# Kernel optimization log

Measured on AMD Instinct MI355X. Metric: run time of the kernel, lower is better.

The kernel has to match this reference:

```python
import jax, jax.numpy as jnp
import numpy as np

B, T, D = 2, 1024, 2048      # batch, seq, model dim
E, F, K = 64, 512, 4          # n_experts, expert hidden, top-k
S, HS = 2, 512 * 4            # shared experts, shared hidden = expert_dim * topk


def setup_inputs() -> dict:
    key = jax.random.key(0)
    ks = jax.random.split(key, 9)
    s = 0.02
    f32 = jnp.float32
    return {
        "x": jax.random.normal(ks[0], (B, T, D), f32),
        "router_w": jax.random.normal(ks[1], (D, E), f32) * s,
        "router_bias": jnp.zeros((E,), f32),
        "wg": jax.random.normal(ks[2], (E, D, F), f32) * s,
        "wu": jax.random.normal(ks[3], (E, D, F), f32) * s,
        "wd": jax.random.normal(ks[4], (E, F, D), f32) * s,
        "swg": jax.random.normal(ks[5], (S, D, HS), f32) * s,
        "swu": jax.random.normal(ks[6], (S, D, HS), f32) * s,
        "swd": jax.random.normal(ks[7], (S, HS, D), f32) * s,
    }


def reference(x, router_w, router_bias, wg, wu, wd, swg, swu, swd):
    b, t, d = x.shape
    flat = x.reshape(b * t, d)                      # [N, D]
    n = flat.shape[0]

    # Router: softmax scores, top-k selection on (logits + bias)
    logits = flat @ router_w                         # [N, E]
    scores = jax.nn.softmax(logits, axis=-1)
    _, topk_idx = jax.lax.top_k(logits + router_bias, K)          # [N, K]
    topk_scores = jnp.take_along_axis(scores, topk_idx, axis=-1)  # [N, K]
    topk_scores = topk_scores / topk_scores.sum(axis=-1, keepdims=True)

    # Dense combine weights: w[n, e] = normalized score if expert e selected else 0
    comb = jnp.zeros((n, E), dtype=flat.dtype).at[
        jnp.arange(n)[:, None], topk_idx].set(topk_scores)        # [N, E]

    # Routed experts (SwiGLU), computed densely and masked by combine weights
    g = jax.nn.silu(jnp.einsum('nd,edf->nef', flat, wg))          # [N, E, F]
    u = jnp.einsum('nd,edf->nef', flat, wu)                       # [N, E, F]
    routed = jnp.einsum('ne,nef,efd->nd', comb, g * u, wd)        # [N, D]

    # Shared experts (always active, summed)
    sg = jax.nn.silu(jnp.einsum('nd,sdh->nsh', flat, swg))        # [N, S, HS]
    su = jnp.einsum('nd,sdh->nsh', flat, swu)
    shared = jnp.einsum('nsh,shd->nd', sg * su, swd)              # [N, D]

    return (routed + shared).reshape(b, t, d)
```

## Files before the change

kernel.cpp:

```cpp
#include <hip/hip_runtime.h>
#include <hip/hip_bf16.h>

typedef __bf16 bf16x8 __attribute__((ext_vector_type(8)));
typedef float f32x4 __attribute__((ext_vector_type(4)));
typedef unsigned short u16x4 __attribute__((ext_vector_type(4)));
typedef unsigned short u16x8 __attribute__((ext_vector_type(8)));

#define DEVI __device__ __forceinline__

constexpr int N_TOK = 2048;
constexpr int DIM   = 2048;
constexpr int NEXP  = 64;
constexpr int FDIM  = 512;
constexpr int TOPK  = 4;
constexpr int NSH   = 2;
constexpr int HSH   = 2048;

#define WAIT_VM0 asm volatile("s_waitcnt vmcnt(0)" ::: "memory")
#define WAIT_VM3 asm volatile("s_waitcnt vmcnt(3)" ::: "memory")
#define WAIT_VM4 asm volatile("s_waitcnt vmcnt(4)" ::: "memory")
#define WAIT_VM6 asm volatile("s_waitcnt vmcnt(6)" ::: "memory")
#define WAIT_LG0 asm volatile("s_waitcnt lgkmcnt(0)" ::: "memory")
#define SBAR __builtin_amdgcn_s_barrier()

DEVI unsigned short f2b(float f) {
  union { float fv; unsigned u; } v; v.fv = f;
  unsigned r = v.u + 0x7fffu + ((v.u >> 16) & 1u);
  return (unsigned short)(r >> 16);
}
DEVI float b2f(unsigned short h) {
  union { unsigned u; float f; } v; v.u = ((unsigned)h) << 16;
  return v.f;
}
DEVI void gll16(const void* g, void* l) {
  __builtin_amdgcn_global_load_lds((const __attribute__((address_space(1))) unsigned*)g,
                                   (__attribute__((address_space(3))) unsigned*)l, 16, 0, 0);
}
DEVI unsigned cvtpk(float lo, float hi) {
  unsigned r;
  asm("v_cvt_pk_bf16_f32 %0, %1, %2" : "=v"(r) : "v"(lo), "v"(hi));
  return r;
}
DEVI bf16x8 fragB(const float* base, int str) {
  union { unsigned u[4]; bf16x8 v; } r;
  #pragma unroll
  for (int p = 0; p < 4; ++p) r.u[p] = cvtpk(base[(2 * p) * str], base[(2 * p + 1) * str]);
  return r.v;
}

__global__ void cvt_x_kernel(const float* __restrict__ x, unsigned short* __restrict__ xb) {
  const size_t i = ((size_t)blockIdx.x * 256 + threadIdx.x) * 8;
  const float4 a = *reinterpret_cast<const float4*>(x + i);
  const float4 b = *reinterpret_cast<const float4*>(x + i + 4);
  u16x8 o;
  o[0] = f2b(a.x); o[1] = f2b(a.y); o[2] = f2b(a.z); o[3] = f2b(a.w);
  o[4] = f2b(b.x); o[5] = f2b(b.y); o[6] = f2b(b.z); o[7] = f2b(b.w);
  *reinterpret_cast<u16x8*>(xb + i) = o;
}

__global__ __launch_bounds__(256)
void tr_shared_kernel(const float* __restrict__ swu, const float* __restrict__ swg,
                      const float* __restrict__ swd, unsigned short* __restrict__ swuT,
                      unsigned short* __restrict__ swgT, unsigned short* __restrict__ swdT) {
  __shared__ float Lf[64][68];
  const int tid = threadIdx.x;
  const int r0 = blockIdx.x * 64, c0 = blockIdx.y * 64;
  const int z = blockIdx.z, mat = z >> 1;
  const size_t soff = (size_t)(z & 1) * DIM * HSH;
  const float* in = (mat == 0 ? swu : mat == 1 ? swg : swd) + soff;
  unsigned short* ot = (mat == 0 ? swuT : mat == 1 ? swgT : swdT) + soff;
  #pragma unroll
  for (int j = 0; j < 4; ++j) {
    const int idx = j * 1024 + tid * 4;
    const int row = idx >> 6, col = idx & 63;
    const float4 v = *reinterpret_cast<const float4*>(in + (size_t)(r0 + row) * 2048 + c0 + col);
    *reinterpret_cast<float4*>(&Lf[row][col]) = v;
  }
  __syncthreads();
  #pragma unroll
  for (int j = 0; j < 4; ++j) {
    const int idx = j * 1024 + tid * 4;
    const int orow = idx >> 6, ocol = idx & 63;
    u16x4 o;
    o[0] = f2b(Lf[ocol][orow]);     o[1] = f2b(Lf[ocol + 1][orow]);
    o[2] = f2b(Lf[ocol + 2][orow]); o[3] = f2b(Lf[ocol + 3][orow]);
    *reinterpret_cast<u16x4*>(ot + (size_t)(c0 + orow) * 2048 + r0 + ocol) = o;
  }
}

__global__ __launch_bounds__(256)
void router_kernel(const float* __restrict__ x, const float* __restrict__ rw,
                   const float* __restrict__ rb, int* __restrict__ cnt,
                   int* __restrict__ listTok, float* __restrict__ listW,
                   int* __restrict__ tokEP) {
  __shared__ float Lx[8][128];
  const int tid = threadIdx.x;
  const int lane = tid & 63;
  const int wave = tid >> 6;
  const int tokBase = blockIdx.x * 8;

  float acc0 = 0.f, acc1 = 0.f;
  for (int dc = 0; dc < DIM; dc += 128) {
    __syncthreads();
    {
      const int idx = tid * 4;
      const int row = idx >> 7, col = idx & 127;
      *reinterpret_cast<float4*>(&Lx[row][col]) =
          *reinterpret_cast<const float4*>(x + (size_t)(tokBase + row) * DIM + dc + col);
    }
    __syncthreads();
    #pragma unroll 16
    for (int dd = 0; dd < 128; ++dd) {
      const float r = rw[(size_t)(dc + dd) * NEXP + lane];
      acc0 = fmaf(Lx[wave * 2 + 0][dd], r, acc0);
      acc1 = fmaf(Lx[wave * 2 + 1][dd], r, acc1);
    }
  }

  const float bias = rb[lane];
  #pragma unroll
  for (int t = 0; t < 2; ++t) {
    const float v = (t == 0) ? acc0 : acc1;
    const int token = tokBase + wave * 2 + t;
    float m = v;
    #pragma unroll
    for (int o = 32; o > 0; o >>= 1) m = fmaxf(m, __shfl_xor(m, o));
    const float p = expf(v - m);
    float ss = p;
    #pragma unroll
    for (int o = 32; o > 0; o >>= 1) ss += __shfl_xor(ss, o);
    const float score = p / ss;
    float cur = v + bias;
    float wk[TOPK]; int ik[TOPK]; float wsum = 0.f;
    #pragma unroll
    for (int k = 0; k < TOPK; ++k) {
      float tm = cur;
      #pragma unroll
      for (int o = 32; o > 0; o >>= 1) tm = fmaxf(tm, __shfl_xor(tm, o));
      const unsigned long long msk = __ballot(cur == tm);
      const int sel = (int)__builtin_ctzll(msk);
      const float w = __shfl(score, sel);
      wk[k] = w; ik[k] = sel; wsum += w;
      if (lane == sel) cur = -3.4e38f;
    }
    if (lane < TOPK) {
      const int e = ik[lane];
      const float w = wk[lane] / wsum;
      const int slot = atomicAdd(&cnt[e], 1);
      listTok[(size_t)e * N_TOK + slot] = token;
      listW[(size_t)e * N_TOK + slot] = w;
      tokEP[token * TOPK + lane] = (e << 16) | slot;
    }
  }
}

__global__ void scan_kernel(const int* __restrict__ cnt, int* __restrict__ off) {
  if (threadIdx.x == 0) {
    int s = 0;
    for (int e = 0; e < NEXP; ++e) { off[e] = s; s += cnt[e]; }
  }
}

__global__ __launch_bounds__(256, 3)
void up_routed(const unsigned short* __restrict__ xb,
               const float* __restrict__ Wu, const float* __restrict__ Wg,
               const int* __restrict__ cnt, const int* __restrict__ off,
               const int* __restrict__ listTok, const float* __restrict__ listW,
               unsigned short* __restrict__ H) {
  constexpr int NT = DIM / 32;
  const int tid = threadIdx.x;
  const int f0 = blockIdx.x * 64;
  const int e  = blockIdx.y;
  const int m0 = blockIdx.z * 128;
  const int c = cnt[e];
  if (m0 >= c) return;
  const int rcnt = min(128, c - m0);
  const int rowbase = off[e] + m0;

  __shared__ __align__(16) unsigned short Al[2][4][128][8];
  __shared__ __align__(16) float Bf[2][2][32][64];
  __shared__ float wSs[128];

  if (tid < 128) wSs[tid] = (tid < rcnt) ? listW[(size_t)e * N_TOK + m0 + tid] : 0.f;
  WAIT_LG0;

  const int wid = tid >> 6, l = tid & 63;
  const int wm = wid >> 1, wn = wid & 1;
  const int lc = l & 15, hi = l >> 4;

  const int t0 = listTok[(size_t)e * N_TOK + m0 + min(l, rcnt - 1)];
  const int t1 = listTok[(size_t)e * N_TOK + m0 + min(64 + l, rcnt - 1)];
  const unsigned short* pa0 = xb + (size_t)t0 * DIM;
  const unsigned short* pa1 = xb + (size_t)t1 * DIM;
  const unsigned short* pas = (wid & 1) ? pa1 : pa0;
  const float* pbu = Wu + (size_t)e * DIM * FDIM + (size_t)(l >> 4) * FDIM + f0 + (l & 15) * 4;
  const float* pbg = Wg + (size_t)e * DIM * FDIM + (size_t)(l >> 4) * FDIM + f0 + (l & 15) * 4;

  auto stage = [&](int g, int b) {
    const int d0 = g * 32;
    gll16(pas + d0 + (wid >> 1) * 8,      &Al[b][wid >> 1][(wid & 1) * 64][0]);
    gll16(pas + d0 + (wid >> 1) * 8 + 16, &Al[b][(wid >> 1) + 2][(wid & 1) * 64][0]);
    gll16(pbu + (size_t)(d0 + 4 * wid) * FDIM,      &Bf[b][0][4 * wid][0]);
    gll16(pbu + (size_t)(d0 + 4 * wid + 16) * FDIM, &Bf[b][0][4 * wid + 16][0]);
    gll16(pbg + (size_t)(d0 + 4 * wid) * FDIM,      &Bf[b][1][4 * wid][0]);
    gll16(pbg + (size_t)(d0 + 4 * wid + 16) * FDIM, &Bf[b][1][4 * wid + 16][0]);
  };

  f32x4 aU[4][2], aG[4][2];
  #pragma unroll
  for (int i = 0; i < 4; ++i)
    #pragma unroll
    for (int j = 0; j < 2; ++j) { aU[i][j] = f32x4{0,0,0,0}; aG[i][j] = f32x4{0,0,0,0}; }

  stage(0, 0);
  for (int g = 0; g < NT; ++g) {
    const int b = g & 1;
    if (g + 1 < NT) { stage(g + 1, b ^ 1); WAIT_VM6; } else { WAIT_VM0; }
    SBAR;
    bf16x8 af[4];
    #pragma unroll
    for (int mi = 0; mi < 4; ++mi)
      af[mi] = *reinterpret_cast<const bf16x8*>(&Al[b][hi][wm * 64 + mi * 16 + lc][0]);
    #pragma unroll
    for (int ni = 0; ni < 2; ++ni) {
      const bf16x8 bu = fragB(&Bf[b][0][hi * 8][wn * 32 + ni * 16 + lc], 64);
      const bf16x8 bg = fragB(&Bf[b][1][hi * 8][wn * 32 + ni * 16 + lc], 64);
      #pragma unroll
      for (int mi = 0; mi < 4; ++mi) {
        aU[mi][ni] = __builtin_amdgcn_mfma_f32_16x16x32_bf16(af[mi], bu, aU[mi][ni], 0, 0, 0);
        aG[mi][ni] = __builtin_amdgcn_mfma_f32_16x16x32_bf16(af[mi], bg, aG[mi][ni], 0, 0, 0);
      }
    }
    SBAR;
  }

  #pragma unroll
  for (int mi = 0; mi < 4; ++mi)
    #pragma unroll
    for (int ni = 0; ni < 2; ++ni)
      #pragma unroll
      for (int r2 = 0; r2 < 4; ++r2) {
        const int row = wm * 64 + mi * 16 + hi * 4 + r2;
        if (row < rcnt) {
          const int col = f0 + wn * 32 + ni * 16 + lc;
          const float g = aG[mi][ni][r2], u = aU[mi][ni][r2];
          const float h = (g / (1.f + __expf(-g))) * u * wSs[row];
          H[(size_t)(rowbase + row) * FDIM + col] = f2b(h);
        }
      }
}

__global__ __launch_bounds__(256, 3)
void down_routed(const unsigned short* __restrict__ Hr, const float* __restrict__ wd,
                 const int* __restrict__ cnt, const int* __restrict__ off,
                 unsigned short* __restrict__ P) {
  constexpr int NT = FDIM / 32;
  const int tid = threadIdx.x;
  const int x0 = blockIdx.x * 128;
  const int e  = blockIdx.y;
  const int m0 = blockIdx.z * 128;
  const int c = cnt[e];
  if (m0 >= c) return;
  const int rcnt = min(128, c - m0);
  const int rowbase = off[e] + m0;

  __shared__ __align__(16) unsigned short Al[2][4][128][8];
  __shared__ __align__(16) float Bf[2][32][128];

  const int wid = tid >> 6, l = tid & 63;
  const int wm = wid >> 1, wn = wid & 1;
  const int lc = l & 15, hi = l >> 4;

  const unsigned short* pa0 = Hr + (size_t)(rowbase + min(l, rcnt - 1)) * FDIM;
  const unsigned short* pa1 = Hr + (size_t)(rowbase + min(64 + l, rcnt - 1)) * FDIM;
  const unsigned short* pas = (wid & 1) ? pa1 : pa0;
  const float* pB = wd + (size_t)e * FDIM * DIM + (size_t)(l >> 5) * DIM + x0 + (l & 31) * 4;

  auto stage = [&](int g, int b) {
    const int d0 = g * 32;
    gll16(pas + d0 + (wid >> 1) * 8,      &Al[b][wid >> 1][(wid & 1) * 64][0]);
    gll16(pas + d0 + (wid >> 1) * 8 + 16, &Al[b][(wid >> 1) + 2][(wid & 1) * 64][0]);
    #pragma unroll
    for (int cc = 0; cc < 4; ++cc) {
      const int i = cc * 4 + wid;
      gll16(pB + (size_t)(d0 + 2 * i) * DIM, &Bf[b][2 * i][0]);
    }
  };

  f32x4 acc[4][4];
  #pragma unroll
  for (int i = 0; i < 4; ++i)
    #pragma unroll
    for (int j = 0; j < 4; ++j) acc[i][j] = f32x4{0,0,0,0};

  stage(0, 0);
  for (int g = 0; g < NT; ++g) {
    const int b = g & 1;
    if (g + 1 < NT) { stage(g + 1, b ^ 1); WAIT_VM6; } else { WAIT_VM0; }
    SBAR;
    bf16x8 af[4];
    #pragma unroll
    for (int mi = 0; mi < 4; ++mi)
      af[mi] = *reinterpret_cast<const bf16x8*>(&Al[b][hi][wm * 64 + mi * 16 + lc][0]);
    #pragma unroll
    for (int ni = 0; ni < 4; ++ni) {
      const bf16x8 bq = fragB(&Bf[b][hi * 8][wn * 64 + ni * 16 + lc], 128);
      #pragma unroll
      for (int mi = 0; mi < 4; ++mi)
        acc[mi][ni] = __builtin_amdgcn_mfma_f32_16x16x32_bf16(af[mi], bq, acc[mi][ni], 0, 0, 0);
    }
    SBAR;
  }

  #pragma unroll
  for (int mi = 0; mi < 4; ++mi)
    #pragma unroll
    for (int ni = 0; ni < 4; ++ni)
      #pragma unroll
      for (int r2 = 0; r2 < 4; ++r2) {
        const int row = wm * 64 + mi * 16 + hi * 4 + r2;
        if (row < rcnt) {
          const int col = x0 + wn * 64 + ni * 16 + lc;
          P[(size_t)(rowbase + row) * DIM + col] = f2b(acc[mi][ni][r2]);
        }
      }
}

__global__ __launch_bounds__(256, 4)
void up_shared(const unsigned short* __restrict__ xb,
               const unsigned short* __restrict__ WuT, const unsigned short* __restrict__ WgT,
               unsigned short* __restrict__ H) {
  constexpr int NT = DIM / 32;
  const int tid = threadIdx.x;
  const int f0 = blockIdx.x * 64;
  const int s  = blockIdx.y;
  const int m0 = blockIdx.z * 128;

  __shared__ __align__(16) unsigned short Al[2][4][128][8];
  __shared__ __align__(16) unsigned short Bu[2][4][64][8];
  __shared__ __align__(16) unsigned short Bg[2][4][64][8];

  const int wid = tid >> 6, l = tid & 63;
  const int wm = wid >> 1, wn = wid & 1;
  const int lc = l & 15, hi = l >> 4;

  const unsigned short* pa0 = xb + (size_t)(m0 + l) * DIM;
  const unsigned short* pa1 = xb + (size_t)(m0 + 64 + l) * DIM;
  const unsigned short* pas = (wid & 1) ? pa1 : pa0;
  const unsigned short* pbu = WuT + (size_t)s * HSH * DIM + (size_t)(f0 + l) * DIM;
  const unsigned short* pbg = WgT + (size_t)s * HSH * DIM + (size_t)(f0 + l) * DIM;

  auto stage = [&](int g, int b) {
    const int d0 = g * 32;
    gll16(pas + d0 + (wid >> 1) * 8,      &Al[b][wid >> 1][(wid & 1) * 64][0]);
    gll16(pas + d0 + (wid >> 1) * 8 + 16, &Al[b][(wid >> 1) + 2][(wid & 1) * 64][0]);
    gll16(pbu + d0 + wid * 8, &Bu[b][wid][0][0]);
    gll16(pbg + d0 + wid * 8, &Bg[b][wid][0][0]);
  };

  f32x4 aU[4][2], aG[4][2];
  #pragma unroll
  for (int i = 0; i < 4; ++i)
    #pragma unroll
    for (int j = 0; j < 2; ++j) { aU[i][j] = f32x4{0,0,0,0}; aG[i][j] = f32x4{0,0,0,0}; }

  stage(0, 0);
  for (int g = 0; g < NT; ++g) {
    const int b = g & 1;
    if (g + 1 < NT) { stage(g + 1, b ^ 1); WAIT_VM4; } else { WAIT_VM0; }
    SBAR;
    bf16x8 af[4], bu[2], bg[2];
    #pragma unroll
    for (int mi = 0; mi < 4; ++mi)
      af[mi] = *reinterpret_cast<const bf16x8*>(&Al[b][hi][wm * 64 + mi * 16 + lc][0]);
    #pragma unroll
    for (int ni = 0; ni < 2; ++ni) {
      bu[ni] = *reinterpret_cast<const bf16x8*>(&Bu[b][hi][wn * 32 + ni * 16 + lc][0]);
      bg[ni] = *reinterpret_cast<const bf16x8*>(&Bg[b][hi][wn * 32 + ni * 16 + lc][0]);
    }
    #pragma unroll
    for (int mi = 0; mi < 4; ++mi)
      #pragma unroll
      for (int ni = 0; ni < 2; ++ni) {
        aU[mi][ni] = __builtin_amdgcn_mfma_f32_16x16x32_bf16(af[mi], bu[ni], aU[mi][ni], 0, 0, 0);
        aG[mi][ni] = __builtin_amdgcn_mfma_f32_16x16x32_bf16(af[mi], bg[ni], aG[mi][ni], 0, 0, 0);
      }
    SBAR;
  }

  #pragma unroll
  for (int mi = 0; mi < 4; ++mi)
    #pragma unroll
    for (int ni = 0; ni < 2; ++ni)
      #pragma unroll
      for (int r2 = 0; r2 < 4; ++r2) {
        const int row = wm * 64 + mi * 16 + hi * 4 + r2;
        const int col = f0 + wn * 32 + ni * 16 + lc;
        const float g = aG[mi][ni][r2], u = aU[mi][ni][r2];
        H[((size_t)s * N_TOK + m0 + row) * HSH + col] = f2b((g / (1.f + __expf(-g))) * u);
      }
}

__global__ __launch_bounds__(256, 4)
void down_shared(const unsigned short* __restrict__ Hs, const unsigned short* __restrict__ swdT,
                 float* __restrict__ out) {
  constexpr int NT = 2 * HSH / 32;
  const int tid = threadIdx.x;
  const int x0 = blockIdx.x * 128;
  const int m0 = blockIdx.z * 64;

  __shared__ __align__(16) unsigned short Al[2][4][64][8];
  __shared__ __align__(16) unsigned short Bl[2][4][128][8];

  const int wid = tid >> 6, l = tid & 63;
  const int wm = wid >> 1, wn = wid & 1;
  const int lc = l & 15, hi = l >> 4;

  const unsigned short* paA = Hs + (size_t)(m0 + l) * HSH;
  const unsigned short* pb0 = swdT + (size_t)(x0 + l) * HSH;
  const unsigned short* pb1 = swdT + (size_t)(x0 + 64 + l) * HSH;
  const unsigned short* pbs = (wid & 1) ? pb1 : pb0;

  auto stage = [&](int g, int b) {
    const int seg = g >> 6;
    const int dk = (g & 63) * 32;
    const size_t aoff = (size_t)seg * N_TOK * HSH;
    const size_t boff = (size_t)seg * HSH * DIM;
    gll16(paA + aoff + dk + wid * 8, &Al[b][wid][0][0]);
    gll16(pbs + boff + dk + (wid >> 1) * 8,      &Bl[b][wid >> 1][(wid & 1) * 64][0]);
    gll16(pbs + boff + dk + (wid >> 1) * 8 + 16, &Bl[b][(wid >> 1) + 2][(wid & 1) * 64][0]);
  };

  f32x4 acc[2][4];
  #pragma unroll
  for (int i = 0; i < 2; ++i)
    #pragma unroll
    for (int j = 0; j < 4; ++j) acc[i][j] = f32x4{0,0,0,0};

  stage(0, 0);
  for (int g = 0; g < NT; ++g) {
    const int b = g & 1;
    if (g + 1 < NT) { stage(g + 1, b ^ 1); WAIT_VM3; } else { WAIT_VM0; }
    SBAR;
    bf16x8 af[2], bq[4];
    #pragma unroll
    for (int mi = 0; mi < 2; ++mi)
      af[mi] = *reinterpret_cast<const bf16x8*>(&Al[b][hi][wm * 32 + mi * 16 + lc][0]);
    #pragma unroll
    for (int ni = 0; ni < 4; ++ni)
      bq[ni] = *reinterpret_cast<const bf16x8*>(&Bl[b][hi][wn * 64 + ni * 16 + lc][0]);
    #pragma unroll
    for (int mi = 0; mi < 2; ++mi)
      #pragma unroll
      for (int ni = 0; ni < 4; ++ni)
        acc[mi][ni] = __builtin_amdgcn_mfma_f32_16x16x32_bf16(af[mi], bq[ni], acc[mi][ni], 0, 0, 0);
    SBAR;
  }

  #pragma unroll
  for (int mi = 0; mi < 2; ++mi)
    #pragma unroll
    for (int ni = 0; ni < 4; ++ni)
      #pragma unroll
      for (int r2 = 0; r2 < 4; ++r2) {
        const int row = wm * 32 + mi * 16 + hi * 4 + r2;
        const int col = x0 + wn * 64 + ni * 16 + lc;
        out[(size_t)(m0 + row) * DIM + col] = acc[mi][ni][r2];
      }
}

__global__ __launch_bounds__(256)
void combine_kernel(const int* __restrict__ tokEP, const int* __restrict__ off,
                    const unsigned short* __restrict__ P, float* __restrict__ out) {
  const int n = blockIdx.x;
  const int tid = threadIdx.x;
  int rows[4];
  #pragma unroll
  for (int k = 0; k < TOPK; ++k) {
    const int ep = tokEP[n * TOPK + k];
    rows[k] = off[ep >> 16] + (ep & 0xffff);
  }
  const int cc = tid * 8;
  float* po = out + (size_t)n * DIM + cc;
  float4 o0 = *reinterpret_cast<const float4*>(po);
  float4 o1 = *reinterpret_cast<const float4*>(po + 4);
  #pragma unroll
  for (int k = 0; k < TOPK; ++k) {
    const u16x8 v = *reinterpret_cast<const u16x8*>(P + (size_t)rows[k] * DIM + cc);
    o0.x += b2f(v[0]); o0.y += b2f(v[1]); o0.z += b2f(v[2]); o0.w += b2f(v[3]);
    o1.x += b2f(v[4]); o1.y += b2f(v[5]); o1.z += b2f(v[6]); o1.w += b2f(v[7]);
  }
  *reinterpret_cast<float4*>(po) = o0;
  *reinterpret_cast<float4*>(po + 4) = o1;
}

extern "C" void kernel_launch(void* const* d_in, const int* in_sizes, int n_in,
                              void* d_out, int out_size, void* d_ws, size_t ws_size,
                              hipStream_t stream) {
  const float* x   = (const float*)d_in[0];
  const float* rw  = (const float*)d_in[1];
  const float* rb  = (const float*)d_in[2];
  const float* wg  = (const float*)d_in[3];
  const float* wu  = (const float*)d_in[4];
  const float* wd  = (const float*)d_in[5];
  const float* swg = (const float*)d_in[6];
  const float* swu = (const float*)d_in[7];
  const float* swd = (const float*)d_in[8];
  float* out = (float*)d_out;
  char* ws = (char*)d_ws;

  int* cnt = (int*)ws;
  int* off = (int*)(ws + 256);
  int* tokEP = (int*)(ws + 4096);
  int* listTok = (int*)(ws + 64 * 1024);
  float* listW = (float*)(ws + 576 * 1024);
  unsigned short* xb   = (unsigned short*)(ws + (size_t) 2 * 1024 * 1024);
  unsigned short* Hr   = (unsigned short*)(ws + (size_t)10 * 1024 * 1024);
  unsigned short* Hs   = (unsigned short*)(ws + (size_t)18 * 1024 * 1024);
  unsigned short* swuT = (unsigned short*)(ws + (size_t)34 * 1024 * 1024);
  unsigned short* swgT = (unsigned short*)(ws + (size_t)50 * 1024 * 1024);
  unsigned short* swdT = (unsigned short*)(ws + (size_t)66 * 1024 * 1024);
  unsigned short* P    = (unsigned short*)(ws + (size_t)82 * 1024 * 1024);

  hipMemsetAsync(cnt, 0, NEXP * sizeof(int), stream);
  cvt_x_kernel<<<(N_TOK * DIM) / (256 * 8), 256, 0, stream>>>(x, xb);
  tr_shared_kernel<<<dim3(32, 32, 6), 256, 0, stream>>>(swu, swg, swd, swuT, swgT, swdT);
  router_kernel<<<N_TOK / 8, 256, 0, stream>>>(x, rw, rb, cnt, listTok, listW, tokEP);
  scan_kernel<<<1, 64, 0, stream>>>(cnt, off);

  up_routed<<<dim3(FDIM / 64, NEXP, 16), 256, 0, stream>>>(
      xb, wu, wg, cnt, off, listTok, listW, Hr);
  up_shared<<<dim3(HSH / 64, NSH, N_TOK / 128), 256, 0, stream>>>(
      xb, swuT, swgT, Hs);
  down_shared<<<dim3(DIM / 128, 1, N_TOK / 64), 256, 0, stream>>>(
      Hs, swdT, out);
  down_routed<<<dim3(DIM / 128, NEXP, 16), 256, 0, stream>>>(
      Hr, wd, cnt, off, P);
  combine_kernel<<<N_TOK, 256, 0, stream>>>(tokEP, off, P, out);
}
```

Baseline: 717.4 us.

## Restructure routed GEMMs with register-staged bf16 weights and triple-buffer shared GEMMs

The routed up-projection is split into two passes, first up then gate, and each pass covers 256 rows per block so every weight tile is shared by twice as many tokens. The fp32 routed weights are now loaded into registers, converted to bf16 once, and written to LDS. This removes the per-fragment fp32-to-bf16 conversion that ran inside the MFMA loop. The down-routed kernel gets the same treatment with 64-column tiles, and the shared-expert GEMMs switch from double to triple buffering. Kernel launch order also changes. The costs are an extra read-modify-write of H in the gate pass and higher LDS and register pressure.

```diff
diff --git a/kernel.cpp b/kernel.cpp
--- a/kernel.cpp
+++ b/kernel.cpp
@@ -3,6 +3,8 @@
 
 typedef __bf16 bf16x8 __attribute__((ext_vector_type(8)));
 typedef float f32x4 __attribute__((ext_vector_type(4)));
+typedef float f32x2 __attribute__((ext_vector_type(2)));
+typedef unsigned short u16x2 __attribute__((ext_vector_type(2)));
 typedef unsigned short u16x4 __attribute__((ext_vector_type(4)));
 typedef unsigned short u16x8 __attribute__((ext_vector_type(8)));
 
@@ -17,9 +19,11 @@
 constexpr int HSH   = 2048;
 
 #define WAIT_VM0 asm volatile("s_waitcnt vmcnt(0)" ::: "memory")
+#define WAIT_VM2 asm volatile("s_waitcnt vmcnt(2)" ::: "memory")
 #define WAIT_VM3 asm volatile("s_waitcnt vmcnt(3)" ::: "memory")
 #define WAIT_VM4 asm volatile("s_waitcnt vmcnt(4)" ::: "memory")
 #define WAIT_VM6 asm volatile("s_waitcnt vmcnt(6)" ::: "memory")
+#define WAIT_VM8 asm volatile("s_waitcnt vmcnt(8)" ::: "memory")
 #define WAIT_LG0 asm volatile("s_waitcnt lgkmcnt(0)" ::: "memory")
 #define SBAR __builtin_amdgcn_s_barrier()
 
@@ -35,17 +39,6 @@
 DEVI void gll16(const void* g, void* l) {
   __builtin_amdgcn_global_load_lds((const __attribute__((address_space(1))) unsigned*)g,
                                    (__attribute__((address_space(3))) unsigned*)l, 16, 0, 0);
-}
-DEVI unsigned cvtpk(float lo, float hi) {
-  unsigned r;
-  asm("v_cvt_pk_bf16_f32 %0, %1, %2" : "=v"(r) : "v"(lo), "v"(hi));
-  return r;
-}
-DEVI bf16x8 fragB(const float* base, int str) {
-  union { unsigned u[4]; bf16x8 v; } r;
-  #pragma unroll
-  for (int p = 0; p < 4; ++p) r.u[p] = cvtpk(base[(2 * p) * str], base[(2 * p + 1) * str]);
-  return r.v;
 }
 
 __global__ void cvt_x_kernel(const float* __restrict__ x, unsigned short* __restrict__ xb) {
@@ -161,9 +154,9 @@
   }
 }
 
+template<bool GPASS>
 __global__ __launch_bounds__(256, 3)
-void up_routed(const unsigned short* __restrict__ xb,
-               const float* __restrict__ Wu, const float* __restrict__ Wg,
+void up_routed(const unsigned short* __restrict__ xb, const float* __restrict__ W,
                const int* __restrict__ cnt, const int* __restrict__ off,
                const int* __restrict__ listTok, const float* __restrict__ listW,
                unsigned short* __restrict__ H) {
@@ -171,83 +164,127 @@
   const int tid = threadIdx.x;
   const int f0 = blockIdx.x * 64;
   const int e  = blockIdx.y;
-  const int m0 = blockIdx.z * 128;
+  const int m0 = blockIdx.z * 256;
   const int c = cnt[e];
   if (m0 >= c) return;
-  const int rcnt = min(128, c - m0);
+  const int rc0 = min(128, c - m0);
+  const int rc1 = min(128, max(0, c - m0 - 128));
   const int rowbase = off[e] + m0;
 
-  __shared__ __align__(16) unsigned short Al[2][4][128][8];
-  __shared__ __align__(16) float Bf[2][2][32][64];
-  __shared__ float wSs[128];
-
-  if (tid < 128) wSs[tid] = (tid < rcnt) ? listW[(size_t)e * N_TOK + m0 + tid] : 0.f;
-  WAIT_LG0;
+  __shared__ __align__(16) unsigned short Al[2][2][4][128][8];
+  __shared__ __align__(16) unsigned short Bb[2][4][64][8];
+  __shared__ float wSs[256];
+
+  if (GPASS) wSs[tid] = (m0 + tid < c) ? listW[(size_t)e * N_TOK + m0 + tid] : 0.f;
 
   const int wid = tid >> 6, l = tid & 63;
   const int wm = wid >> 1, wn = wid & 1;
   const int lc = l & 15, hi = l >> 4;
 
-  const int t0 = listTok[(size_t)e * N_TOK + m0 + min(l, rcnt - 1)];
-  const int t1 = listTok[(size_t)e * N_TOK + m0 + min(64 + l, rcnt - 1)];
-  const unsigned short* pa0 = xb + (size_t)t0 * DIM;
-  const unsigned short* pa1 = xb + (size_t)t1 * DIM;
-  const unsigned short* pas = (wid & 1) ? pa1 : pa0;
-  const float* pbu = Wu + (size_t)e * DIM * FDIM + (size_t)(l >> 4) * FDIM + f0 + (l & 15) * 4;
-  const float* pbg = Wg + (size_t)e * DIM * FDIM + (size_t)(l >> 4) * FDIM + f0 + (l & 15) * 4;
-
-  auto stage = [&](int g, int b) {
-    const int d0 = g * 32;
-    gll16(pas + d0 + (wid >> 1) * 8,      &Al[b][wid >> 1][(wid & 1) * 64][0]);
-    gll16(pas + d0 + (wid >> 1) * 8 + 16, &Al[b][(wid >> 1) + 2][(wid & 1) * 64][0]);
-    gll16(pbu + (size_t)(d0 + 4 * wid) * FDIM,      &Bf[b][0][4 * wid][0]);
-    gll16(pbu + (size_t)(d0 + 4 * wid + 16) * FDIM, &Bf[b][0][4 * wid + 16][0]);
-    gll16(pbg + (size_t)(d0 + 4 * wid) * FDIM,      &Bf[b][1][4 * wid][0]);
-    gll16(pbg + (size_t)(d0 + 4 * wid + 16) * FDIM, &Bf[b][1][4 * wid + 16][0]);
-  };
-
-  f32x4 aU[4][2], aG[4][2];
+  const unsigned short* pa[4];
+  #pragma unroll
+  for (int j = 0; j < 4; ++j) {
+    const int tok = listTok[(size_t)e * N_TOK + min(m0 + j * 64 + l, c - 1)];
+    pa[j] = xb + (size_t)tok * DIM;
+  }
+  const float* pw = W + (size_t)e * DIM * FDIM + f0 + (tid & 15) * 4;
+  const int ko = tid >> 4;
+
+  f32x4 rb0[2], rb1[2];
+  f32x4 a0[4][2], a1[4][2];
   #pragma unroll
   for (int i = 0; i < 4; ++i)
     #pragma unroll
-    for (int j = 0; j < 2; ++j) { aU[i][j] = f32x4{0,0,0,0}; aG[i][j] = f32x4{0,0,0,0}; }
-
-  stage(0, 0);
-  for (int g = 0; g < NT; ++g) {
-    const int b = g & 1;
-    if (g + 1 < NT) { stage(g + 1, b ^ 1); WAIT_VM6; } else { WAIT_VM0; }
-    SBAR;
-    bf16x8 af[4];
+    for (int j = 0; j < 2; ++j) { a0[i][j] = f32x4{0,0,0,0}; a1[i][j] = f32x4{0,0,0,0}; }
+
+#define UPR_STAGEA(G, B_) do { const int d0_ = (G) * 32;            \
+    gll16(pa[0] + d0_ + wid * 8, &Al[B_][0][wid][0][0]);            \
+    gll16(pa[1] + d0_ + wid * 8, &Al[B_][0][wid][64][0]);           \
+    gll16(pa[2] + d0_ + wid * 8, &Al[B_][1][wid][0][0]);            \
+    gll16(pa[3] + d0_ + wid * 8, &Al[B_][1][wid][64][0]); } while (0)
+
+#define UPR_LOADB(G, R) do { const int d0_ = (G) * 32;                                    \
+    R[0] = *reinterpret_cast<const f32x4*>(pw + (size_t)(d0_ + 2 * ko) * FDIM);           \
+    R[1] = *reinterpret_cast<const f32x4*>(pw + (size_t)(d0_ + 2 * ko + 1) * FDIM); } while (0)
+
+#define UPR_WRITEB(R, B_) do {                                                            \
+    _Pragma("unroll")                                                                     \
+    for (int cc = 0; cc < 4; ++cc) {                                                      \
+      u16x2 v2; v2[0] = f2b(R[0][cc]); v2[1] = f2b(R[1][cc]);                             \
+      *reinterpret_cast<u16x2*>(&Bb[B_][ko >> 2][(tid & 15) * 4 + cc][2 * (ko & 3)]) = v2;\
+    } } while (0)
+
+#define UPR_COMPUTE(B_) do {                                                              \
+    const bf16x8 bq0 = *reinterpret_cast<const bf16x8*>(&Bb[B_][hi][wn * 32 + lc][0]);    \
+    const bf16x8 bq1 = *reinterpret_cast<const bf16x8*>(&Bb[B_][hi][wn * 32 + 16 + lc][0]);\
+    _Pragma("unroll")                                                                     \
+    for (int mi = 0; mi < 4; ++mi) {                                                      \
+      const bf16x8 af = *reinterpret_cast<const bf16x8*>(&Al[B_][0][hi][wm * 64 + mi * 16 + lc][0]); \
+      a0[mi][0] = __builtin_amdgcn_mfma_f32_16x16x32_bf16(af, bq0, a0[mi][0], 0, 0, 0);   \
+      a0[mi][1] = __builtin_amdgcn_mfma_f32_16x16x32_bf16(af, bq1, a0[mi][1], 0, 0, 0);   \
+    }                                                                                     \
+    _Pragma("unroll")                                                                     \
+    for (int mi = 0; mi < 4; ++mi) {                                                      \
+      const bf16x8 af = *reinterpret_cast<const bf16x8*>(&Al[B_][1][hi][wm * 64 + mi * 16 + lc][0]); \
+      a1[mi][0] = __builtin_amdgcn_mfma_f32_16x16x32_bf16(af, bq0, a1[mi][0], 0, 0, 0);   \
+      a1[mi][1] = __builtin_amdgcn_mfma_f32_16x16x32_bf16(af, bq1, a1[mi][1], 0, 0, 0);   \
+    } } while (0)
+
+  UPR_LOADB(0, rb0);
+  UPR_STAGEA(0, 0);
+  UPR_LOADB(1, rb1);
+  WAIT_VM6;
+  UPR_WRITEB(rb0, 0);
+  WAIT_VM2;
+  WAIT_LG0; SBAR;
+
+  for (int t = 0; t < NT - 2; t += 2) {
+    UPR_STAGEA(t + 1, 1);
+    UPR_LOADB(t + 2, rb0);
+    WAIT_VM6; UPR_WRITEB(rb1, 1);
+    UPR_COMPUTE(0);
+    WAIT_VM2; WAIT_LG0; SBAR;
+    UPR_STAGEA(t + 2, 0);
+    UPR_LOADB(t + 3, rb1);
+    WAIT_VM6; UPR_WRITEB(rb0, 0);
+    UPR_COMPUTE(1);
+    WAIT_VM2; WAIT_LG0; SBAR;
+  }
+  UPR_STAGEA(NT - 1, 1);
+  WAIT_VM4;
+  UPR_WRITEB(rb1, 1);
+  UPR_COMPUTE(0);
+  WAIT_VM0; WAIT_LG0; SBAR;
+  UPR_COMPUTE(1);
+
+#undef UPR_STAGEA
+#undef UPR_LOADB
+#undef UPR_WRITEB
+#undef UPR_COMPUTE
+
+  #pragma unroll
+  for (int tile = 0; tile < 2; ++tile) {
+    const int rc = tile ? rc1 : rc0;
     #pragma unroll
     for (int mi = 0; mi < 4; ++mi)
-      af[mi] = *reinterpret_cast<const bf16x8*>(&Al[b][hi][wm * 64 + mi * 16 + lc][0]);
-    #pragma unroll
-    for (int ni = 0; ni < 2; ++ni) {
-      const bf16x8 bu = fragB(&Bf[b][0][hi * 8][wn * 32 + ni * 16 + lc], 64);
-      const bf16x8 bg = fragB(&Bf[b][1][hi * 8][wn * 32 + ni * 16 + lc], 64);
       #pragma unroll
-      for (int mi = 0; mi < 4; ++mi) {
-        aU[mi][ni] = __builtin_amdgcn_mfma_f32_16x16x32_bf16(af[mi], bu, aU[mi][ni], 0, 0, 0);
-        aG[mi][ni] = __builtin_amdgcn_mfma_f32_16x16x32_bf16(af[mi], bg, aG[mi][ni], 0, 0, 0);
-      }
-    }
-    SBAR;
-  }
-
-  #pragma unroll
-  for (int mi = 0; mi < 4; ++mi)
-    #pragma unroll
-    for (int ni = 0; ni < 2; ++ni)
-      #pragma unroll
-      for (int r2 = 0; r2 < 4; ++r2) {
-        const int row = wm * 64 + mi * 16 + hi * 4 + r2;
-        if (row < rcnt) {
-          const int col = f0 + wn * 32 + ni * 16 + lc;
-          const float g = aG[mi][ni][r2], u = aU[mi][ni][r2];
-          const float h = (g / (1.f + __expf(-g))) * u * wSs[row];
-          H[(size_t)(rowbase + row) * FDIM + col] = f2b(h);
+      for (int ni = 0; ni < 2; ++ni)
+        #pragma unroll
+        for (int r2 = 0; r2 < 4; ++r2) {
+          const int row = wm * 64 + mi * 16 + hi * 4 + r2;
+          if (row < rc) {
+            const int col = f0 + wn * 32 + ni * 16 + lc;
+            const size_t idx = (size_t)(rowbase + tile * 128 + row) * FDIM + col;
+            const float v = tile ? a1[mi][ni][r2] : a0[mi][ni][r2];
+            if (GPASS) {
+              const float u = b2f(H[idx]);
+              H[idx] = f2b((v / (1.f + __expf(-v))) * u * wSs[tile * 128 + row]);
+            } else {
+              H[idx] = f2b(v);
+            }
+          }
         }
-      }
+  }
 }
 
 __global__ __launch_bounds__(256, 3)
@@ -256,77 +293,124 @@
                  unsigned short* __restrict__ P) {
   constexpr int NT = FDIM / 32;
   const int tid = threadIdx.x;
-  const int x0 = blockIdx.x * 128;
+  const int x0 = blockIdx.x * 64;
   const int e  = blockIdx.y;
-  const int m0 = blockIdx.z * 128;
+  const int m0 = blockIdx.z * 256;
   const int c = cnt[e];
   if (m0 >= c) return;
-  const int rcnt = min(128, c - m0);
+  const int rc0 = min(128, c - m0);
+  const int rc1 = min(128, max(0, c - m0 - 128));
   const int rowbase = off[e] + m0;
 
-  __shared__ __align__(16) unsigned short Al[2][4][128][8];
-  __shared__ __align__(16) float Bf[2][32][128];
+  __shared__ __align__(16) unsigned short Al[2][2][4][128][8];
+  __shared__ __align__(16) unsigned short Bb[2][4][64][8];
 
   const int wid = tid >> 6, l = tid & 63;
   const int wm = wid >> 1, wn = wid & 1;
   const int lc = l & 15, hi = l >> 4;
 
-  const unsigned short* pa0 = Hr + (size_t)(rowbase + min(l, rcnt - 1)) * FDIM;
-  const unsigned short* pa1 = Hr + (size_t)(rowbase + min(64 + l, rcnt - 1)) * FDIM;
-  const unsigned short* pas = (wid & 1) ? pa1 : pa0;
-  const float* pB = wd + (size_t)e * FDIM * DIM + (size_t)(l >> 5) * DIM + x0 + (l & 31) * 4;
-
-  auto stage = [&](int g, int b) {
-    const int d0 = g * 32;
-    gll16(pas + d0 + (wid >> 1) * 8,      &Al[b][wid >> 1][(wid & 1) * 64][0]);
-    gll16(pas + d0 + (wid >> 1) * 8 + 16, &Al[b][(wid >> 1) + 2][(wid & 1) * 64][0]);
-    #pragma unroll
-    for (int cc = 0; cc < 4; ++cc) {
-      const int i = cc * 4 + wid;
-      gll16(pB + (size_t)(d0 + 2 * i) * DIM, &Bf[b][2 * i][0]);
-    }
-  };
-
-  f32x4 acc[4][4];
+  const unsigned short* pa[4];
+  #pragma unroll
+  for (int j = 0; j < 4; ++j)
+    pa[j] = Hr + (size_t)(rowbase + min(j * 64 + l, c - m0 - 1)) * FDIM;
+
+  const float* pw = wd + (size_t)e * FDIM * DIM + x0 + (tid & 31) * 2;
+  const int ko = tid >> 5;
+
+  f32x2 rb0[4], rb1[4];
+  f32x4 a0[4][2], a1[4][2];
   #pragma unroll
   for (int i = 0; i < 4; ++i)
     #pragma unroll
-    for (int j = 0; j < 4; ++j) acc[i][j] = f32x4{0,0,0,0};
-
-  stage(0, 0);
-  for (int g = 0; g < NT; ++g) {
-    const int b = g & 1;
-    if (g + 1 < NT) { stage(g + 1, b ^ 1); WAIT_VM6; } else { WAIT_VM0; }
-    SBAR;
-    bf16x8 af[4];
+    for (int j = 0; j < 2; ++j) { a0[i][j] = f32x4{0,0,0,0}; a1[i][j] = f32x4{0,0,0,0}; }
+
+#define DNR_STAGEA(G, B_) do { const int d0_ = (G) * 32;            \
+    gll16(pa[0] + d0_ + wid * 8, &Al[B_][0][wid][0][0]);            \
+    gll16(pa[1] + d0_ + wid * 8, &Al[B_][0][wid][64][0]);           \
+    gll16(pa[2] + d0_ + wid * 8, &Al[B_][1][wid][0][0]);            \
+    gll16(pa[3] + d0_ + wid * 8, &Al[B_][1][wid][64][0]); } while (0)
+
+#define DNR_LOADB(G, R) do { const int d0_ = (G) * 32;                                    \
+    _Pragma("unroll")                                                                     \
+    for (int j = 0; j < 4; ++j)                                                           \
+      R[j] = *reinterpret_cast<const f32x2*>(pw + (size_t)(d0_ + 4 * ko + j) * DIM); } while (0)
+
+#define DNR_WRITEB(R, B_) do {                                                            \
+    _Pragma("unroll")                                                                     \
+    for (int cc = 0; cc < 2; ++cc) {                                                      \
+      u16x4 v4; v4[0] = f2b(R[0][cc]); v4[1] = f2b(R[1][cc]);                             \
+      v4[2] = f2b(R[2][cc]); v4[3] = f2b(R[3][cc]);                                       \
+      *reinterpret_cast<u16x4*>(&Bb[B_][ko >> 1][(tid & 31) * 2 + cc][4 * (ko & 1)]) = v4;\
+    } } while (0)
+
+#define DNR_COMPUTE(B_) do {                                                              \
+    const bf16x8 bq0 = *reinterpret_cast<const bf16x8*>(&Bb[B_][hi][wn * 32 + lc][0]);    \
+    const bf16x8 bq1 = *reinterpret_cast<const bf16x8*>(&Bb[B_][hi][wn * 32 + 16 + lc][0]);\
+    _Pragma("unroll")                                                                     \
+    for (int mi = 0; mi < 4; ++mi) {                                                      \
+      const bf16x8 af = *reinterpret_cast<const bf16x8*>(&Al[B_][0][hi][wm * 64 + mi * 16 + lc][0]); \
+      a0[mi][0] = __builtin_amdgcn_mfma_f32_16x16x32_bf16(af, bq0, a0[mi][0], 0, 0, 0);   \
+      a0[mi][1] = __builtin_amdgcn_mfma_f32_16x16x32_bf16(af, bq1, a0[mi][1], 0, 0, 0);   \
+    }                                                                                     \
+    _Pragma("unroll")                                                                     \
+    for (int mi = 0; mi < 4; ++mi) {                                                      \
+      const bf16x8 af = *reinterpret_cast<const bf16x8*>(&Al[B_][1][hi][wm * 64 + mi * 16 + lc][0]); \
+      a1[mi][0] = __builtin_amdgcn_mfma_f32_16x16x32_bf16(af, bq0, a1[mi][0], 0, 0, 0);   \
+      a1[mi][1] = __builtin_amdgcn_mfma_f32_16x16x32_bf16(af, bq1, a1[mi][1], 0, 0, 0);   \
+    } } while (0)
+
+  DNR_LOADB(0, rb0);
+  DNR_STAGEA(0, 0);
+  DNR_LOADB(1, rb1);
+  WAIT_VM8;
+  DNR_WRITEB(rb0, 0);
+  WAIT_VM4;
+  WAIT_LG0; SBAR;
+
+  for (int t = 0; t < NT - 2; t += 2) {
+    DNR_STAGEA(t + 1, 1);
+    DNR_LOADB(t + 2, rb0);
+    WAIT_VM8; DNR_WRITEB(rb1, 1);
+    DNR_COMPUTE(0);
+    WAIT_VM4; WAIT_LG0; SBAR;
+    DNR_STAGEA(t + 2, 0);
+    DNR_LOADB(t + 3, rb1);
+    WAIT_VM8; DNR_WRITEB(rb0, 0);
+    DNR_COMPUTE(1);
+    WAIT_VM4; WAIT_LG0; SBAR;
+  }
+  DNR_STAGEA(NT - 1, 1);
+  WAIT_VM4;
+  DNR_WRITEB(rb1, 1);
+  DNR_COMPUTE(0);
+  WAIT_VM0; WAIT_LG0; SBAR;
+  DNR_COMPUTE(1);
+
+#undef DNR_STAGEA
+#undef DNR_LOADB
+#undef DNR_WRITEB
+#undef DNR_COMPUTE
+
+  #pragma unroll
+  for (int tile = 0; tile < 2; ++tile) {
+    const int rc = tile ? rc1 : rc0;
     #pragma unroll
     for (int mi = 0; mi < 4; ++mi)
-      af[mi] = *reinterpret_cast<const bf16x8*>(&Al[b][hi][wm * 64 + mi * 16 + lc][0]);
-    #pragma unroll
-    for (int ni = 0; ni < 4; ++ni) {
-      const bf16x8 bq = fragB(&Bf[b][hi * 8][wn * 64 + ni * 16 + lc], 128);
       #pragma unroll
-      for (int mi = 0; mi < 4; ++mi)
-        acc[mi][ni] = __builtin_amdgcn_mfma_f32_16x16x32_bf16(af[mi], bq, acc[mi][ni], 0, 0, 0);
-    }
-    SBAR;
-  }
-
-  #pragma unroll
-  for (int mi = 0; mi < 4; ++mi)
-    #pragma unroll
-    for (int ni = 0; ni < 4; ++ni)
-      #pragma unroll
-      for (int r2 = 0; r2 < 4; ++r2) {
-        const int row = wm * 64 + mi * 16 + hi * 4 + r2;
-        if (row < rcnt) {
-          const int col = x0 + wn * 64 + ni * 16 + lc;
-          P[(size_t)(rowbase + row) * DIM + col] = f2b(acc[mi][ni][r2]);
+      for (int ni = 0; ni < 2; ++ni)
+        #pragma unroll
+        for (int r2 = 0; r2 < 4; ++r2) {
+          const int row = wm * 64 + mi * 16 + hi * 4 + r2;
+          if (row < rc) {
+            const int col = x0 + wn * 32 + ni * 16 + lc;
+            const float v = tile ? a1[mi][ni][r2] : a0[mi][ni][r2];
+            P[(size_t)(rowbase + tile * 128 + row) * DIM + col] = f2b(v);
+          }
         }
-      }
-}
-
-__global__ __launch_bounds__(256, 4)
+  }
+}
+
+__global__ __launch_bounds__(256, 3)
 void up_shared(const unsigned short* __restrict__ xb,
                const unsigned short* __restrict__ WuT, const unsigned short* __restrict__ WgT,
                unsigned short* __restrict__ H) {
@@ -336,9 +420,9 @@
   const int s  = blockIdx.y;
   const int m0 = blockIdx.z * 128;
 
-  __shared__ __align__(16) unsigned short Al[2][4][128][8];
-  __shared__ __align__(16) unsigned short Bu[2][4][64][8];
-  __shared__ __align__(16) unsigned short Bg[2][4][64][8];
+  __shared__ __align__(16) unsigned short Al[3][4][128][8];
+  __shared__ __align__(16) unsigned short Bu[3][4][64][8];
+  __shared__ __align__(16) unsigned short Bg[3][4][64][8];
 
   const int wid = tid >> 6, l = tid & 63;
   const int wm = wid >> 1, wn = wid & 1;
@@ -346,37 +430,31 @@
 
   const unsigned short* pa0 = xb + (size_t)(m0 + l) * DIM;
   const unsigned short* pa1 = xb + (size_t)(m0 + 64 + l) * DIM;
-  const unsigned short* pas = (wid & 1) ? pa1 : pa0;
   const unsigned short* pbu = WuT + (size_t)s * HSH * DIM + (size_t)(f0 + l) * DIM;
   const unsigned short* pbg = WgT + (size_t)s * HSH * DIM + (size_t)(f0 + l) * DIM;
 
-  auto stage = [&](int g, int b) {
+  f32x4 aU[4][2], aG[4][2];
+  #pragma unroll
+  for (int i = 0; i < 4; ++i)
+    #pragma unroll
+    for (int j = 0; j < 2; ++j) { aU[i][j] = f32x4{0,0,0,0}; aG[i][j] = f32x4{0,0,0,0}; }
+
+  auto stage = [&](int g, int bb) {
     const int d0 = g * 32;
-    gll16(pas + d0 + (wid >> 1) * 8,      &Al[b][wid >> 1][(wid & 1) * 64][0]);
-    gll16(pas + d0 + (wid >> 1) * 8 + 16, &Al[b][(wid >> 1) + 2][(wid & 1) * 64][0]);
-    gll16(pbu + d0 + wid * 8, &Bu[b][wid][0][0]);
-    gll16(pbg + d0 + wid * 8, &Bg[b][wid][0][0]);
+    gll16(pa0 + d0 + wid * 8, &Al[bb][wid][0][0]);
+    gll16(pa1 + d0 + wid * 8, &Al[bb][wid][64][0]);
+    gll16(pbu + d0 + wid * 8, &Bu[bb][wid][0][0]);
+    gll16(pbg + d0 + wid * 8, &Bg[bb][wid][0][0]);
   };
-
-  f32x4 aU[4][2], aG[4][2];
-  #pragma unroll
-  for (int i = 0; i < 4; ++i)
-    #pragma unroll
-    for (int j = 0; j < 2; ++j) { aU[i][j] = f32x4{0,0,0,0}; aG[i][j] = f32x4{0,0,0,0}; }
-
-  stage(0, 0);
-  for (int g = 0; g < NT; ++g) {
-    const int b = g & 1;
-    if (g + 1 < NT) { stage(g + 1, b ^ 1); WAIT_VM4; } else { WAIT_VM0; }
-    SBAR;
+  auto compute = [&](int bb) {
     bf16x8 af[4], bu[2], bg[2];
     #pragma unroll
     for (int mi = 0; mi < 4; ++mi)
-      af[mi] = *reinterpret_cast<const bf16x8*>(&Al[b][hi][wm * 64 + mi * 16 + lc][0]);
+      af[mi] = *reinterpret_cast<const bf16x8*>(&Al[bb][hi][wm * 64 + mi * 16 + lc][0]);
     #pragma unroll
     for (int ni = 0; ni < 2; ++ni) {
-      bu[ni] = *reinterpret_cast<const bf16x8*>(&Bu[b][hi][wn * 32 + ni * 16 + lc][0]);
-      bg[ni] = *reinterpret_cast<const bf16x8*>(&Bg[b][hi][wn * 32 + ni * 16 + lc][0]);
+      bu[ni] = *reinterpret_cast<const bf16x8*>(&Bu[bb][hi][wn * 32 + ni * 16 + lc][0]);
+      bg[ni] = *reinterpret_cast<const bf16x8*>(&Bg[bb][hi][wn * 32 + ni * 16 + lc][0]);
     }
     #pragma unroll
     for (int mi = 0; mi < 4; ++mi)
@@ -385,8 +463,22 @@
         aU[mi][ni] = __builtin_amdgcn_mfma_f32_16x16x32_bf16(af[mi], bu[ni], aU[mi][ni], 0, 0, 0);
         aG[mi][ni] = __builtin_amdgcn_mfma_f32_16x16x32_bf16(af[mi], bg[ni], aG[mi][ni], 0, 0, 0);
       }
-    SBAR;
-  }
+  };
+
+  stage(0, 0); stage(1, 1);
+  WAIT_VM4; SBAR;
+  int cur = 0, fut = 2;
+  for (int t = 0; t < NT - 2; ++t) {
+    stage(t + 2, fut);
+    compute(cur);
+    WAIT_VM4; SBAR;
+    cur = (cur == 2) ? 0 : cur + 1;
+    fut = (fut == 2) ? 0 : fut + 1;
+  }
+  compute(cur);
+  WAIT_VM0; SBAR;
+  cur = (cur == 2) ? 0 : cur + 1;
+  compute(cur);
 
   #pragma unroll
   for (int mi = 0; mi < 4; ++mi)
@@ -409,8 +501,8 @@
   const int x0 = blockIdx.x * 128;
   const int m0 = blockIdx.z * 64;
 
-  __shared__ __align__(16) unsigned short Al[2][4][64][8];
-  __shared__ __align__(16) unsigned short Bl[2][4][128][8];
+  __shared__ __align__(16) unsigned short Al[3][4][64][8];
+  __shared__ __align__(16) unsigned short Bl[3][4][128][8];
 
   const int wid = tid >> 6, l = tid & 63;
   const int wm = wid >> 1, wn = wid & 1;
@@ -419,43 +511,51 @@
   const unsigned short* paA = Hs + (size_t)(m0 + l) * HSH;
   const unsigned short* pb0 = swdT + (size_t)(x0 + l) * HSH;
   const unsigned short* pb1 = swdT + (size_t)(x0 + 64 + l) * HSH;
-  const unsigned short* pbs = (wid & 1) ? pb1 : pb0;
-
-  auto stage = [&](int g, int b) {
+
+  f32x4 acc[2][4];
+  #pragma unroll
+  for (int i = 0; i < 2; ++i)
+    #pragma unroll
+    for (int j = 0; j < 4; ++j) acc[i][j] = f32x4{0,0,0,0};
+
+  auto stage = [&](int g, int bb) {
     const int seg = g >> 6;
     const int dk = (g & 63) * 32;
     const size_t aoff = (size_t)seg * N_TOK * HSH;
     const size_t boff = (size_t)seg * HSH * DIM;
-    gll16(paA + aoff + dk + wid * 8, &Al[b][wid][0][0]);
-    gll16(pbs + boff + dk + (wid >> 1) * 8,      &Bl[b][wid >> 1][(wid & 1) * 64][0]);
-    gll16(pbs + boff + dk + (wid >> 1) * 8 + 16, &Bl[b][(wid >> 1) + 2][(wid & 1) * 64][0]);
+    gll16(paA + aoff + dk + wid * 8, &Al[bb][wid][0][0]);
+    gll16(pb0 + boff + dk + wid * 8, &Bl[bb][wid][0][0]);
+    gll16(pb1 + boff + dk + wid * 8, &Bl[bb][wid][64][0]);
   };
-
-  f32x4 acc[2][4];
-  #pragma unroll
-  for (int i = 0; i < 2; ++i)
-    #pragma unroll
-    for (int j = 0; j < 4; ++j) acc[i][j] = f32x4{0,0,0,0};
-
-  stage(0, 0);
-  for (int g = 0; g < NT; ++g) {
-    const int b = g & 1;
-    if (g + 1 < NT) { stage(g + 1, b ^ 1); WAIT_VM3; } else { WAIT_VM0; }
-    SBAR;
+  auto compute = [&](int bb) {
     bf16x8 af[2], bq[4];
     #pragma unroll
     for (int mi = 0; mi < 2; ++mi)
-      af[mi] = *reinterpret_cast<const bf16x8*>(&Al[b][hi][wm * 32 + mi * 16 + lc][0]);
+      af[mi] = *reinterpret_cast<const bf16x8*>(&Al[bb][hi][wm * 32 + mi * 16 + lc][0]);
     #pragma unroll
     for (int ni = 0; ni < 4; ++ni)
-      bq[ni] = *reinterpret_cast<const bf16x8*>(&Bl[b][hi][wn * 64 + ni * 16 + lc][0]);
+      bq[ni] = *reinterpret_cast<const bf16x8*>(&Bl[bb][hi][wn * 64 + ni * 16 + lc][0]);
     #pragma unroll
     for (int mi = 0; mi < 2; ++mi)
       #pragma unroll
       for (int ni = 0; ni < 4; ++ni)
         acc[mi][ni] = __builtin_amdgcn_mfma_f32_16x16x32_bf16(af[mi], bq[ni], acc[mi][ni], 0, 0, 0);
-    SBAR;
-  }
+  };
+
+  stage(0, 0); stage(1, 1);
+  WAIT_VM3; SBAR;
+  int cur = 0, fut = 2;
+  for (int t = 0; t < NT - 2; ++t) {
+    stage(t + 2, fut);
+    compute(cur);
+    WAIT_VM3; SBAR;
+    cur = (cur == 2) ? 0 : cur + 1;
+    fut = (fut == 2) ? 0 : fut + 1;
+  }
+  compute(cur);
+  WAIT_VM0; SBAR;
+  cur = (cur == 2) ? 0 : cur + 1;
+  compute(cur);
 
   #pragma unroll
   for (int mi = 0; mi < 2; ++mi)
@@ -524,17 +624,14 @@
 
   hipMemsetAsync(cnt, 0, NEXP * sizeof(int), stream);
   cvt_x_kernel<<<(N_TOK * DIM) / (256 * 8), 256, 0, stream>>>(x, xb);
-  tr_shared_kernel<<<dim3(32, 32, 6), 256, 0, stream>>>(swu, swg, swd, swuT, swgT, swdT);
   router_kernel<<<N_TOK / 8, 256, 0, stream>>>(x, rw, rb, cnt, listTok, listW, tokEP);
   scan_kernel<<<1, 64, 0, stream>>>(cnt, off);
-
-  up_routed<<<dim3(FDIM / 64, NEXP, 16), 256, 0, stream>>>(
-      xb, wu, wg, cnt, off, listTok, listW, Hr);
-  up_shared<<<dim3(HSH / 64, NSH, N_TOK / 128), 256, 0, stream>>>(
-      xb, swuT, swgT, Hs);
-  down_shared<<<dim3(DIM / 128, 1, N_TOK / 64), 256, 0, stream>>>(
-      Hs, swdT, out);
-  down_routed<<<dim3(DIM / 128, NEXP, 16), 256, 0, stream>>>(
-      Hr, wd, cnt, off, P);
+  tr_shared_kernel<<<dim3(32, 32, 6), 256, 0, stream>>>(swu, swg, swd, swuT, swgT, swdT);
+
+  up_routed<false><<<dim3(8, 64, 8), 256, 0, stream>>>(xb, wu, cnt, off, listTok, listW, Hr);
+  up_routed<true ><<<dim3(8, 64, 8), 256, 0, stream>>>(xb, wg, cnt, off, listTok, listW, Hr);
+  up_shared<<<dim3(32, 2, 16), 256, 0, stream>>>(xb, swuT, swgT, Hs);
+  down_routed<<<dim3(32, 64, 8), 256, 0, stream>>>(Hr, wd, cnt, off, P);
+  down_shared<<<dim3(16, 1, 32), 256, 0, stream>>>(Hs, swdT, out);
   combine_kernel<<<N_TOK, 256, 0, stream>>>(tokEP, off, P, out);
 }
```

Result: slower. 734.2 us (median of 2 runs) (+2.3%).
